# Kernel tuning notes

Measured on AMD Instinct MI355X. Metric: run time of the kernel, lower is better.

The kernel has to match this reference:

```python
import jax, jax.numpy as jnp
import numpy as np

NUM_GRAPHS = 8
N_NODES = 100000


def setup_inputs() -> dict:
    key = jax.random.key(0)
    ks = jax.random.split(key, 8)
    d = 64
    E = 1600000
    x = jax.random.normal(ks[0], (N_NODES, d), dtype=jnp.float32)
    # nn.Linear weights (out,in) with std=0.1 init per GNNlayer; biases zero
    W1 = 0.1 * jax.random.normal(ks[1], (d, d), dtype=jnp.float32)
    W2 = 0.1 * jax.random.normal(ks[2], (d, d), dtype=jnp.float32)
    W3 = 0.1 * jax.random.normal(ks[3], (d, d), dtype=jnp.float32)
    b1 = jnp.zeros((d,), dtype=jnp.float32)
    b2 = jnp.zeros((d,), dtype=jnp.float32)
    b3 = jnp.zeros((d,), dtype=jnp.float32)
    src = jax.random.randint(ks[4], (E,), 0, N_NODES, dtype=jnp.int32)
    dst = jax.random.randint(ks[5], (E,), 0, N_NODES, dtype=jnp.int32)
    node2graph = jnp.sort(jax.random.randint(ks[6], (N_NODES,), 0, NUM_GRAPHS, dtype=jnp.int32))
    return {"x": x, "W1": W1, "b1": b1, "W2": W2, "b2": b2,
            "W3": W3, "b3": b3, "src": src, "dst": dst, "node2graph": node2graph}


def _gnn_layer(h, W, b, src, dst):
    # GNNlayer: per-node linear, then copy_u -> sum reduce at dst
    m = h @ W.T + b                       # [N, d]
    msg = m[src]                          # [E, d] edge gather
    return jax.ops.segment_sum(msg, dst, num_segments=N_NODES)  # [N, d]


def reference(x, W1, b1, W2, b2, W3, b3, src, dst, node2graph):
    h = jnp.tanh(_gnn_layer(x, W1, b1, src, dst))
    h = jnp.tanh(_gnn_layer(h, W2, b2, src, dst))
    H_feat = _gnn_layer(h, W3, b3, src, dst)      # [N, out_dim]
    # dgl.unbatch + per-graph sum of all node features -> scalar per graph
    node_scalar = jnp.sum(H_feat, axis=-1)        # [N]
    per_graph = jax.ops.segment_sum(node_scalar, node2graph, num_segments=NUM_GRAPHS)
    return per_graph[None, :]                     # [1, num_graphs]
```

## Files before the change

kernel.cpp:

```cpp
#include <hip/hip_runtime.h>
#include <math.h>

#define NGRAPHS 8
#define KBSHIFT 8
#define BSZ 256
#define KMAX 512
#define BSTRIDE 6144
#define PCHUNK 3125

typedef _Float16 h2 __attribute__((ext_vector_type(2)));
typedef _Float16 v8hf __attribute__((ext_vector_type(8)));
typedef float f32x4 __attribute__((ext_vector_type(4)));

__device__ __forceinline__ h2 as_h2(unsigned u) { return __builtin_bit_cast(h2, u); }
__device__ __forceinline__ unsigned as_u(h2 h) { return __builtin_bit_cast(unsigned, h); }
__device__ __forceinline__ unsigned pkf16(float a, float b) {
    auto v = __builtin_amdgcn_cvt_pkrtz(a, b);
    return __builtin_bit_cast(unsigned, v);
}
__device__ __forceinline__ float ftanh(float x) {
    float t = __expf(2.0f * x);
    return 1.0f - 2.0f * __builtin_amdgcn_rcpf(t + 1.0f);
}

template<bool TANH, bool INH, bool ZB>
__global__ __launch_bounds__(256) void gemm_kernel(
    const void* __restrict__ in_, const float* __restrict__ W,
    const float* __restrict__ bias, unsigned* __restrict__ out,
    int* __restrict__ bcursor, int N)
{
    __shared__ union {
        struct { uint4 Wc[512]; uint4 Xc[512]; } s;
        float Cf[64 * 68];
    } u;
    const int t = threadIdx.x;
    const int node0 = blockIdx.x * 64;
    if (ZB && blockIdx.x == 0) { bcursor[t] = 0; bcursor[t + 256] = 0; }

    const float4* W4 = (const float4*)W;
    #pragma unroll
    for (int k = 0; k < 2; ++k) {
        int idx = k * 256 + t;
        int o = idx >> 3, ch = idx & 7;
        float4 w0 = W4[idx * 2];
        float4 w1 = W4[idx * 2 + 1];
        u.s.Wc[o * 8 + (ch ^ (o & 7))] =
            make_uint4(pkf16(w0.x, w0.y), pkf16(w0.z, w0.w),
                       pkf16(w1.x, w1.y), pkf16(w1.z, w1.w));
    }
    if (INH) {
        const uint4* in4 = (const uint4*)in_ + (size_t)node0 * 8;
        #pragma unroll
        for (int k = 0; k < 2; ++k) {
            int idx = k * 256 + t;
            int nl = idx >> 3, ch = idx & 7;
            uint4 v = in4[idx];
            h2 p0 = as_h2(v.x), p1 = as_h2(v.y), p2 = as_h2(v.z), p3 = as_h2(v.w);
            float f0 = (float)p0.x, f1 = (float)p0.y, f2 = (float)p1.x, f3 = (float)p1.y;
            float f4 = (float)p2.x, f5 = (float)p2.y, f6 = (float)p3.x, f7 = (float)p3.y;
            if (TANH) {
                f0 = ftanh(f0); f1 = ftanh(f1); f2 = ftanh(f2); f3 = ftanh(f3);
                f4 = ftanh(f4); f5 = ftanh(f5); f6 = ftanh(f6); f7 = ftanh(f7);
            }
            u.s.Xc[nl * 8 + (ch ^ (nl & 7))] =
                make_uint4(pkf16(f0, f1), pkf16(f2, f3), pkf16(f4, f5), pkf16(f6, f7));
        }
    } else {
        const float4* in4 = (const float4*)in_ + (size_t)node0 * 16;
        #pragma unroll
        for (int k = 0; k < 2; ++k) {
            int idx = k * 256 + t;
            int nl = idx >> 3, ch = idx & 7;
            float4 a0 = make_float4(0.f, 0.f, 0.f, 0.f);
            float4 a1 = make_float4(0.f, 0.f, 0.f, 0.f);
            if (node0 + nl < N) { a0 = in4[idx * 2]; a1 = in4[idx * 2 + 1]; }
            if (TANH) {
                a0.x = ftanh(a0.x); a0.y = ftanh(a0.y); a0.z = ftanh(a0.z); a0.w = ftanh(a0.w);
                a1.x = ftanh(a1.x); a1.y = ftanh(a1.y); a1.z = ftanh(a1.z); a1.w = ftanh(a1.w);
            }
            u.s.Xc[nl * 8 + (ch ^ (nl & 7))] =
                make_uint4(pkf16(a0.x, a0.y), pkf16(a0.z, a0.w),
                           pkf16(a1.x, a1.y), pkf16(a1.z, a1.w));
        }
    }
    __syncthreads();

    const int w = t >> 6, l = t & 63;
    const int lo = l & 15, kb = l >> 4, sx = lo & 7;
    const v8hf* Xv = (const v8hf*)u.s.Xc;
    const v8hf* Wv = (const v8hf*)u.s.Wc;
    const int arow = (w * 16 + lo) * 8;
    v8hf a0 = Xv[arow + (kb ^ sx)];
    v8hf a1 = Xv[arow + ((4 + kb) ^ sx)];
    f32x4 acc[4];
    #pragma unroll
    for (int i = 0; i < 4; ++i) acc[i] = (f32x4){0.f, 0.f, 0.f, 0.f};
    #pragma unroll
    for (int ct = 0; ct < 4; ++ct) {
        const int brow = (ct * 16 + lo) * 8;
        v8hf b0 = Wv[brow + (kb ^ sx)];
        v8hf b1 = Wv[brow + ((4 + kb) ^ sx)];
        acc[ct] = __builtin_amdgcn_mfma_f32_16x16x32_f16(a0, b0, acc[ct], 0, 0, 0);
        acc[ct] = __builtin_amdgcn_mfma_f32_16x16x32_f16(a1, b1, acc[ct], 0, 0, 0);
    }
    __syncthreads();

    #pragma unroll
    for (int ct = 0; ct < 4; ++ct) {
        #pragma unroll
        for (int j = 0; j < 4; ++j)
            u.Cf[(w * 16 + kb * 4 + j) * 68 + ct * 16 + lo] = acc[ct][j];
    }
    __syncthreads();

    {
        const int nl = t >> 2, seg = t & 3;
        if (node0 + nl < N) {
            const float* cp = &u.Cf[nl * 68 + seg * 16];
            float4 c0 = *(const float4*)(cp);
            float4 c1 = *(const float4*)(cp + 4);
            float4 c2 = *(const float4*)(cp + 8);
            float4 c3 = *(const float4*)(cp + 12);
            const float4* b4 = (const float4*)bias + seg * 4;
            float4 e0 = b4[0], e1 = b4[1], e2 = b4[2], e3 = b4[3];
            uint4 o0 = make_uint4(pkf16(c0.x + e0.x, c0.y + e0.y), pkf16(c0.z + e0.z, c0.w + e0.w),
                                  pkf16(c1.x + e1.x, c1.y + e1.y), pkf16(c1.z + e1.z, c1.w + e1.w));
            uint4 o1 = make_uint4(pkf16(c2.x + e2.x, c2.y + e2.y), pkf16(c2.z + e2.z, c2.w + e2.w),
                                  pkf16(c3.x + e3.x, c3.y + e3.y), pkf16(c3.z + e3.z, c3.w + e3.w));
            uint4* op = (uint4*)out + (size_t)(node0 + nl) * 8 + seg * 2;
            op[0] = o0;
            op[1] = o1;
        }
    }
}

__global__ __launch_bounds__(512) void partition_kernel(
    const int* __restrict__ src, const int* __restrict__ dst,
    int* __restrict__ bcursor, unsigned* __restrict__ pairs, int E, int K)
{
    __shared__ int h[512];
    __shared__ int sh[512];
    __shared__ int base[512];
    __shared__ int cur[512];
    __shared__ unsigned val[PCHUNK + 3];
    __shared__ unsigned short bk[PCHUNK + 3];
    const int t = threadIdx.x;
    const int lo = blockIdx.x * PCHUNK;
    int hi = lo + PCHUNK; if (hi > E) hi = E;
    const int cnt = hi - lo;

    h[t] = 0; cur[t] = 0;
    __syncthreads();
    for (int e = lo + t; e < hi; e += 512)
        atomicAdd(&h[dst[e] >> KBSHIFT], 1);
    __syncthreads();
    int v = h[t];
    int x = v;
    #pragma unroll
    for (int off = 1; off < 512; off <<= 1) {
        int u = (t >= off) ? h[t - off] : 0;
        __syncthreads();
        x += u;
        h[t] = x;
        __syncthreads();
    }
    sh[t] = x - v;
    base[t] = (t < K && v > 0) ? atomicAdd(&bcursor[t], v) : 0;
    __syncthreads();
    for (int e = lo + t; e < hi; e += 512) {
        int d = dst[e];
        int k = d >> KBSHIFT;
        int pos = atomicAdd(&cur[k], 1);
        int j = sh[k] + pos;
        val[j] = ((unsigned)(d & (BSZ - 1)) << 23) | (unsigned)src[e];
        bk[j] = (unsigned short)k;
    }
    __syncthreads();
    for (int j = t; j < cnt; j += 512) {
        int k = bk[j];
        int idx = base[k] + (j - sh[k]);
        if (idx < BSTRIDE)
            pairs[(size_t)k * BSTRIDE + idx] = val[j];
    }
}

__global__ __launch_bounds__(256) void bucket_build_kernel(
    const unsigned* __restrict__ pairs, const int* __restrict__ bcursor,
    int* __restrict__ rowptr, int* __restrict__ rowend, int* __restrict__ esrc,
    const float* __restrict__ W3, const float* __restrict__ b3,
    float* __restrict__ w3s, int N)
{
    __shared__ int cnt[BSZ];
    __shared__ int tmp[BSZ];
    __shared__ int cur[BSZ];
    const int k = blockIdx.x;
    const int t = threadIdx.x;
    const int ebase = k * BSTRIDE;
    int ec = bcursor[k]; if (ec > BSTRIDE) ec = BSTRIDE;
    const int eend = ebase + ec;

    cnt[t] = 0;
    __syncthreads();
    for (int e = ebase + t; e < eend; e += BSZ)
        atomicAdd(&cnt[pairs[e] >> 23], 1);
    __syncthreads();

    int v = cnt[t];
    tmp[t] = v;
    __syncthreads();
    #pragma unroll
    for (int off = 1; off < BSZ; off <<= 1) {
        int u = (t >= off) ? tmp[t - off] : 0;
        __syncthreads();
        tmp[t] += u;
        __syncthreads();
    }
    int excl = tmp[t] - v;
    cur[t] = excl;
    int n = (k << KBSHIFT) + t;
    if (n < N) {
        rowptr[n] = ebase + excl;
        rowend[n] = ebase + excl + v;
    }
    __syncthreads();

    for (int e = ebase + t; e < eend; e += BSZ) {
        unsigned p = pairs[e];
        int pos = atomicAdd(&cur[p >> 23], 1);
        esrc[ebase + pos] = (int)(p & 0x7fffffu);
    }

    if (k == 0) {
        if (t < 64) {
            float s = 0.f;
            for (int o = 0; o < 64; ++o) s += W3[o * 64 + t];
            w3s[t] = s;
        }
        if (t == 64) {
            float bs = 0.f;
            for (int j = 0; j < 64; ++j) bs += b3[j];
            w3s[64] = bs;
        }
    }
}

__global__ __launch_bounds__(256) void gather_agg_kernel(
    const uint4* __restrict__ m, const int* __restrict__ esrc,
    const int* __restrict__ rowptr, const int* __restrict__ rowend,
    uint4* __restrict__ out, int N)
{
    const int t = threadIdx.x;
    const int n = blockIdx.x * 8 + (t >> 5);
    const int l32 = t & 31;
    const int sub = l32 >> 3, c = l32 & 7;
    h2 a0 = {0, 0}, a1 = {0, 0}, a2 = {0, 0}, a3 = {0, 0};
    if (n < N) {
        int beg = rowptr[n], end = rowend[n];
        int e = beg + sub;
        for (; e + 4 < end; e += 8) {
            int sA = esrc[e], sB = esrc[e + 4];
            uint4 vA = m[(size_t)sA * 8 + c];
            uint4 vB = m[(size_t)sB * 8 + c];
            a0 += as_h2(vA.x); a1 += as_h2(vA.y);
            a2 += as_h2(vA.z); a3 += as_h2(vA.w);
            a0 += as_h2(vB.x); a1 += as_h2(vB.y);
            a2 += as_h2(vB.z); a3 += as_h2(vB.w);
        }
        if (e < end) {
            uint4 vA = m[(size_t)esrc[e] * 8 + c];
            a0 += as_h2(vA.x); a1 += as_h2(vA.y);
            a2 += as_h2(vA.z); a3 += as_h2(vA.w);
        }
    }
    #pragma unroll
    for (int d = 8; d <= 16; d <<= 1) {
        a0 += as_h2(__shfl_xor(as_u(a0), d));
        a1 += as_h2(__shfl_xor(as_u(a1), d));
        a2 += as_h2(__shfl_xor(as_u(a2), d));
        a3 += as_h2(__shfl_xor(as_u(a3), d));
    }
    if (sub == 0 && n < N)
        out[(size_t)n * 8 + c] = make_uint4(as_u(a0), as_u(a1), as_u(a2), as_u(a3));
}

__global__ __launch_bounds__(256) void gather_s3_kernel(
    const uint4* __restrict__ m, const int* __restrict__ esrc,
    const int* __restrict__ rowptr, const int* __restrict__ rowend,
    const float* __restrict__ w3s, float* __restrict__ s3,
    float* __restrict__ outz, int N)
{
    const int t = threadIdx.x;
    if (blockIdx.x == 0 && t < NGRAPHS) outz[t] = 0.f;
    const int n = blockIdx.x * 8 + (t >> 5);
    const int l32 = t & 31;
    const int sub = l32 >> 3, c = l32 & 7;
    h2 a0 = {0, 0}, a1 = {0, 0}, a2 = {0, 0}, a3 = {0, 0};
    if (n < N) {
        int beg = rowptr[n], end = rowend[n];
        int e = beg + sub;
        for (; e + 4 < end; e += 8) {
            int sA = esrc[e], sB = esrc[e + 4];
            uint4 vA = m[(size_t)sA * 8 + c];
            uint4 vB = m[(size_t)sB * 8 + c];
            a0 += as_h2(vA.x); a1 += as_h2(vA.y);
            a2 += as_h2(vA.z); a3 += as_h2(vA.w);
            a0 += as_h2(vB.x); a1 += as_h2(vB.y);
            a2 += as_h2(vB.z); a3 += as_h2(vB.w);
        }
        if (e < end) {
            uint4 vA = m[(size_t)esrc[e] * 8 + c];
            a0 += as_h2(vA.x); a1 += as_h2(vA.y);
            a2 += as_h2(vA.z); a3 += as_h2(vA.w);
        }
    }
    #pragma unroll
    for (int d = 8; d <= 16; d <<= 1) {
        a0 += as_h2(__shfl_xor(as_u(a0), d));
        a1 += as_h2(__shfl_xor(as_u(a1), d));
        a2 += as_h2(__shfl_xor(as_u(a2), d));
        a3 += as_h2(__shfl_xor(as_u(a3), d));
    }
    float4 w0 = ((const float4*)w3s)[c * 2];
    float4 w1 = ((const float4*)w3s)[c * 2 + 1];
    float partial = ftanh((float)a0.x) * w0.x + ftanh((float)a0.y) * w0.y
                  + ftanh((float)a1.x) * w0.z + ftanh((float)a1.y) * w0.w
                  + ftanh((float)a2.x) * w1.x + ftanh((float)a2.y) * w1.y
                  + ftanh((float)a3.x) * w1.z + ftanh((float)a3.y) * w1.w;
    partial += __shfl_xor(partial, 1);
    partial += __shfl_xor(partial, 2);
    partial += __shfl_xor(partial, 4);
    if (l32 == 0 && n < N) s3[n] = partial + w3s[64];
}

__global__ __launch_bounds__(256) void graph_reduce_kernel(
    const float* __restrict__ s3, const int* __restrict__ esrc,
    const int* __restrict__ rowptr, const int* __restrict__ rowend,
    const int* __restrict__ n2g, float* __restrict__ out, int N)
{
    __shared__ float bins[NGRAPHS];
    int t = threadIdx.x;
    if (t < NGRAPHS) bins[t] = 0.f;
    __syncthreads();
    int n = blockIdx.x * 256 + t;
    if (n < N) {
        float acc = 0.f;
        for (int e = rowptr[n]; e < rowend[n]; ++e) acc += s3[esrc[e]];
        atomicAdd(&bins[n2g[n]], acc);
    }
    __syncthreads();
    if (t < NGRAPHS) unsafeAtomicAdd(&out[t], bins[t]);
}

extern "C" void kernel_launch(void* const* d_in, const int* in_sizes, int n_in,
                              void* d_out, int out_size, void* d_ws, size_t ws_size,
                              hipStream_t stream)
{
    const float* x   = (const float*)d_in[0];
    const float* W1  = (const float*)d_in[1];
    const float* b1  = (const float*)d_in[2];
    const float* W2  = (const float*)d_in[3];
    const float* b2  = (const float*)d_in[4];
    const float* W3  = (const float*)d_in[5];
    const float* b3  = (const float*)d_in[6];
    const int*   src = (const int*)d_in[7];
    const int*   dst = (const int*)d_in[8];
    const int*   n2g = (const int*)d_in[9];

    const int N = in_sizes[0] / 64;
    const int E = in_sizes[7];
    const int K = (N + BSZ - 1) >> KBSHIFT;
    const int nb = (N + 255) / 256;

    char* p = (char*)d_ws;
    auto carve = [&](size_t bytes) {
        char* r = p;
        p += (bytes + 255) & ~(size_t)255;
        return r;
    };
    unsigned* A     = (unsigned*)carve((size_t)N * 64 * 2);
    unsigned* B     = (unsigned*)carve((size_t)N * 64 * 2);
    float* s3b      = (float*)carve((size_t)N * sizeof(float));
    float* w3s      = (float*)carve(65 * sizeof(float));
    int*   bcursor  = (int*)carve(KMAX * sizeof(int));
    int*   rowptr   = (int*)carve((size_t)N * sizeof(int));
    int*   rowend   = (int*)carve((size_t)N * sizeof(int));
    int*   esrc     = (int*)carve((size_t)K * BSTRIDE * sizeof(int));
    unsigned* pairs = (unsigned*)B;
    float* out      = (float*)d_out;

    const int gemm_blocks = (N + 63) / 64;
    const int gath_blocks = (N + 7) / 8;
    const int part_blocks = (E + PCHUNK - 1) / PCHUNK;

    gemm_kernel<false, false, true><<<gemm_blocks, 256, 0, stream>>>(x, W1, b1, A, bcursor, N);

    partition_kernel<<<part_blocks, 512, 0, stream>>>(src, dst, bcursor, pairs, E, K);
    bucket_build_kernel<<<K, BSZ, 0, stream>>>(pairs, bcursor, rowptr, rowend,
                                               esrc, W3, b3, w3s, N);

    gather_agg_kernel<<<gath_blocks, 256, 0, stream>>>(
        (const uint4*)A, esrc, rowptr, rowend, (uint4*)B, N);

    gemm_kernel<true, true, false><<<gemm_blocks, 256, 0, stream>>>(B, W2, b2, A, nullptr, N);

    gather_s3_kernel<<<gath_blocks, 256, 0, stream>>>(
        (const uint4*)A, esrc, rowptr, rowend, w3s, s3b, out, N);

    graph_reduce_kernel<<<nb, 256, 0, stream>>>(s3b, esrc, rowptr, rowend, n2g, out, N);
}
```

Baseline: 219.7 us.

## Fuse layer-1 gather-aggregate with layer-2 GEMM and parallelize graph reduce

Merges the edge gather/segment-sum kernel with the following tanh+linear GEMM. Each 64-node block gathers its rows directly into shared memory and then runs the MFMA GEMM, so the fp16 intermediate is never written to and reread from global memory, and one launch is dropped. The final graph reduce now uses 8 lanes per node with shuffle reduction instead of one thread per node. The trade-off is that each fused block processes its 64 nodes in 8 sequential gather rounds, and the grid has fewer blocks than the old gather kernel, which may reduce latency hiding for the random gathers.

```diff
diff --git a/kernel.cpp b/kernel.cpp
--- a/kernel.cpp
+++ b/kernel.cpp
@@ -23,9 +23,9 @@
     return 1.0f - 2.0f * __builtin_amdgcn_rcpf(t + 1.0f);
 }
 
-template<bool TANH, bool INH, bool ZB>
+template<bool TANH, bool ZB>
 __global__ __launch_bounds__(256) void gemm_kernel(
-    const void* __restrict__ in_, const float* __restrict__ W,
+    const float* __restrict__ in_, const float* __restrict__ W,
     const float* __restrict__ bias, unsigned* __restrict__ out,
     int* __restrict__ bcursor, int N)
 {
@@ -48,24 +48,7 @@
             make_uint4(pkf16(w0.x, w0.y), pkf16(w0.z, w0.w),
                        pkf16(w1.x, w1.y), pkf16(w1.z, w1.w));
     }
-    if (INH) {
-        const uint4* in4 = (const uint4*)in_ + (size_t)node0 * 8;
-        #pragma unroll
-        for (int k = 0; k < 2; ++k) {
-            int idx = k * 256 + t;
-            int nl = idx >> 3, ch = idx & 7;
-            uint4 v = in4[idx];
-            h2 p0 = as_h2(v.x), p1 = as_h2(v.y), p2 = as_h2(v.z), p3 = as_h2(v.w);
-            float f0 = (float)p0.x, f1 = (float)p0.y, f2 = (float)p1.x, f3 = (float)p1.y;
-            float f4 = (float)p2.x, f5 = (float)p2.y, f6 = (float)p3.x, f7 = (float)p3.y;
-            if (TANH) {
-                f0 = ftanh(f0); f1 = ftanh(f1); f2 = ftanh(f2); f3 = ftanh(f3);
-                f4 = ftanh(f4); f5 = ftanh(f5); f6 = ftanh(f6); f7 = ftanh(f7);
-            }
-            u.s.Xc[nl * 8 + (ch ^ (nl & 7))] =
-                make_uint4(pkf16(f0, f1), pkf16(f2, f3), pkf16(f4, f5), pkf16(f6, f7));
-        }
-    } else {
+    {
         const float4* in4 = (const float4*)in_ + (size_t)node0 * 16;
         #pragma unroll
         for (int k = 0; k < 2; ++k) {
@@ -134,6 +117,122 @@
     }
 }
 
+__global__ __launch_bounds__(256) void gather_gemm_kernel(
+    const uint4* __restrict__ m, const int* __restrict__ esrc,
+    const int* __restrict__ rowptr, const int* __restrict__ rowend,
+    const float* __restrict__ W, const float* __restrict__ bias,
+    unsigned* __restrict__ out, int N)
+{
+    __shared__ union {
+        struct { uint4 Wc[512]; uint4 Xc[512]; } s;
+        float Cf[64 * 68];
+    } u;
+    const int t = threadIdx.x;
+    const int node0 = blockIdx.x * 64;
+
+    const float4* W4 = (const float4*)W;
+    #pragma unroll
+    for (int k = 0; k < 2; ++k) {
+        int idx = k * 256 + t;
+        int o = idx >> 3, ch = idx & 7;
+        float4 w0 = W4[idx * 2];
+        float4 w1 = W4[idx * 2 + 1];
+        u.s.Wc[o * 8 + (ch ^ (o & 7))] =
+            make_uint4(pkf16(w0.x, w0.y), pkf16(w0.z, w0.w),
+                       pkf16(w1.x, w1.y), pkf16(w1.z, w1.w));
+    }
+
+    const int grp = t >> 5, l32 = t & 31;
+    const int sub = l32 >> 3, c = l32 & 7;
+    for (int i = 0; i < 8; ++i) {
+        const int nl = grp * 8 + i;
+        const int n = node0 + nl;
+        h2 a0 = {0, 0}, a1 = {0, 0}, a2 = {0, 0}, a3 = {0, 0};
+        if (n < N) {
+            int beg = rowptr[n], end = rowend[n];
+            int e = beg + sub;
+            for (; e + 4 < end; e += 8) {
+                int sA = esrc[e], sB = esrc[e + 4];
+                uint4 vA = m[(size_t)sA * 8 + c];
+                uint4 vB = m[(size_t)sB * 8 + c];
+                a0 += as_h2(vA.x); a1 += as_h2(vA.y);
+                a2 += as_h2(vA.z); a3 += as_h2(vA.w);
+                a0 += as_h2(vB.x); a1 += as_h2(vB.y);
+                a2 += as_h2(vB.z); a3 += as_h2(vB.w);
+            }
+            if (e < end) {
+                uint4 vA = m[(size_t)esrc[e] * 8 + c];
+                a0 += as_h2(vA.x); a1 += as_h2(vA.y);
+                a2 += as_h2(vA.z); a3 += as_h2(vA.w);
+            }
+        }
+        #pragma unroll
+        for (int d = 8; d <= 16; d <<= 1) {
+            a0 += as_h2(__shfl_xor(as_u(a0), d));
+            a1 += as_h2(__shfl_xor(as_u(a1), d));
+            a2 += as_h2(__shfl_xor(as_u(a2), d));
+            a3 += as_h2(__shfl_xor(as_u(a3), d));
+        }
+        if (sub == 0) {
+            float f0 = ftanh((float)a0.x), f1 = ftanh((float)a0.y);
+            float f2 = ftanh((float)a1.x), f3 = ftanh((float)a1.y);
+            float f4 = ftanh((float)a2.x), f5 = ftanh((float)a2.y);
+            float f6 = ftanh((float)a3.x), f7 = ftanh((float)a3.y);
+            u.s.Xc[nl * 8 + (c ^ (nl & 7))] =
+                make_uint4(pkf16(f0, f1), pkf16(f2, f3), pkf16(f4, f5), pkf16(f6, f7));
+        }
+    }
+    __syncthreads();
+
+    const int w = t >> 6, l = t & 63;
+    const int lo = l & 15, kb = l >> 4, sx = lo & 7;
+    const v8hf* Xv = (const v8hf*)u.s.Xc;
+    const v8hf* Wv = (const v8hf*)u.s.Wc;
+    const int arow = (w * 16 + lo) * 8;
+    v8hf a0 = Xv[arow + (kb ^ sx)];
+    v8hf a1 = Xv[arow + ((4 + kb) ^ sx)];
+    f32x4 acc[4];
+    #pragma unroll
+    for (int i = 0; i < 4; ++i) acc[i] = (f32x4){0.f, 0.f, 0.f, 0.f};
+    #pragma unroll
+    for (int ct = 0; ct < 4; ++ct) {
+        const int brow = (ct * 16 + lo) * 8;
+        v8hf b0 = Wv[brow + (kb ^ sx)];
+        v8hf b1 = Wv[brow + ((4 + kb) ^ sx)];
+        acc[ct] = __builtin_amdgcn_mfma_f32_16x16x32_f16(a0, b0, acc[ct], 0, 0, 0);
+        acc[ct] = __builtin_amdgcn_mfma_f32_16x16x32_f16(a1, b1, acc[ct], 0, 0, 0);
+    }
+    __syncthreads();
+
+    #pragma unroll
+    for (int ct = 0; ct < 4; ++ct) {
+        #pragma unroll
+        for (int j = 0; j < 4; ++j)
+            u.Cf[(w * 16 + kb * 4 + j) * 68 + ct * 16 + lo] = acc[ct][j];
+    }
+    __syncthreads();
+
+    {
+        const int nl = t >> 2, seg = t & 3;
+        if (node0 + nl < N) {
+            const float* cp = &u.Cf[nl * 68 + seg * 16];
+            float4 c0 = *(const float4*)(cp);
+            float4 c1 = *(const float4*)(cp + 4);
+            float4 c2 = *(const float4*)(cp + 8);
+            float4 c3 = *(const float4*)(cp + 12);
+            const float4* b4 = (const float4*)bias + seg * 4;
+            float4 e0 = b4[0], e1 = b4[1], e2 = b4[2], e3 = b4[3];
+            uint4 o0 = make_uint4(pkf16(c0.x + e0.x, c0.y + e0.y), pkf16(c0.z + e0.z, c0.w + e0.w),
+                                  pkf16(c1.x + e1.x, c1.y + e1.y), pkf16(c1.z + e1.z, c1.w + e1.w));
+            uint4 o1 = make_uint4(pkf16(c2.x + e2.x, c2.y + e2.y), pkf16(c2.z + e2.z, c2.w + e2.w),
+                                  pkf16(c3.x + e3.x, c3.y + e3.y), pkf16(c3.z + e3.z, c3.w + e3.w));
+            uint4* op = (uint4*)out + (size_t)(node0 + nl) * 8 + seg * 2;
+            op[0] = o0;
+            op[1] = o1;
+        }
+    }
+}
+
 __global__ __launch_bounds__(512) void partition_kernel(
     const int* __restrict__ src, const int* __restrict__ dst,
     int* __restrict__ bcursor, unsigned* __restrict__ pairs, int E, int K)
@@ -242,45 +341,6 @@
             w3s[64] = bs;
         }
     }
-}
-
-__global__ __launch_bounds__(256) void gather_agg_kernel(
-    const uint4* __restrict__ m, const int* __restrict__ esrc,
-    const int* __restrict__ rowptr, const int* __restrict__ rowend,
-    uint4* __restrict__ out, int N)
-{
-    const int t = threadIdx.x;
-    const int n = blockIdx.x * 8 + (t >> 5);
-    const int l32 = t & 31;
-    const int sub = l32 >> 3, c = l32 & 7;
-    h2 a0 = {0, 0}, a1 = {0, 0}, a2 = {0, 0}, a3 = {0, 0};
-    if (n < N) {
-        int beg = rowptr[n], end = rowend[n];
-        int e = beg + sub;
-        for (; e + 4 < end; e += 8) {
-            int sA = esrc[e], sB = esrc[e + 4];
-            uint4 vA = m[(size_t)sA * 8 + c];
-            uint4 vB = m[(size_t)sB * 8 + c];
-            a0 += as_h2(vA.x); a1 += as_h2(vA.y);
-            a2 += as_h2(vA.z); a3 += as_h2(vA.w);
-            a0 += as_h2(vB.x); a1 += as_h2(vB.y);
-            a2 += as_h2(vB.z); a3 += as_h2(vB.w);
-        }
-        if (e < end) {
-            uint4 vA = m[(size_t)esrc[e] * 8 + c];
-            a0 += as_h2(vA.x); a1 += as_h2(vA.y);
-            a2 += as_h2(vA.z); a3 += as_h2(vA.w);
-        }
-    }
-    #pragma unroll
-    for (int d = 8; d <= 16; d <<= 1) {
-        a0 += as_h2(__shfl_xor(as_u(a0), d));
-        a1 += as_h2(__shfl_xor(as_u(a1), d));
-        a2 += as_h2(__shfl_xor(as_u(a2), d));
-        a3 += as_h2(__shfl_xor(as_u(a3), d));
-    }
-    if (sub == 0 && n < N)
-        out[(size_t)n * 8 + c] = make_uint4(as_u(a0), as_u(a1), as_u(a2), as_u(a3));
 }
 
 __global__ __launch_bounds__(256) void gather_s3_kernel(
@@ -338,15 +398,20 @@
     const int* __restrict__ n2g, float* __restrict__ out, int N)
 {
     __shared__ float bins[NGRAPHS];
-    int t = threadIdx.x;
+    const int t = threadIdx.x;
     if (t < NGRAPHS) bins[t] = 0.f;
     __syncthreads();
-    int n = blockIdx.x * 256 + t;
+    const int g = t >> 3, c = t & 7;
+    const int n = blockIdx.x * 32 + g;
+    float acc = 0.f;
     if (n < N) {
-        float acc = 0.f;
-        for (int e = rowptr[n]; e < rowend[n]; ++e) acc += s3[esrc[e]];
-        atomicAdd(&bins[n2g[n]], acc);
-    }
+        int beg = rowptr[n], end = rowend[n];
+        for (int e = beg + c; e < end; e += 8) acc += s3[esrc[e]];
+    }
+    acc += __shfl_xor(acc, 1);
+    acc += __shfl_xor(acc, 2);
+    acc += __shfl_xor(acc, 4);
+    if (c == 0 && n < N) atomicAdd(&bins[n2g[n]], acc);
     __syncthreads();
     if (t < NGRAPHS) unsafeAtomicAdd(&out[t], bins[t]);
 }
@@ -369,7 +434,7 @@
     const int N = in_sizes[0] / 64;
     const int E = in_sizes[7];
     const int K = (N + BSZ - 1) >> KBSHIFT;
-    const int nb = (N + 255) / 256;
+    const int nb = (N + 31) / 32;
 
     char* p = (char*)d_ws;
     auto carve = [&](size_t bytes) {
@@ -392,19 +457,17 @@
     const int gath_blocks = (N + 7) / 8;
     const int part_blocks = (E + PCHUNK - 1) / PCHUNK;
 
-    gemm_kernel<false, false, true><<<gemm_blocks, 256, 0, stream>>>(x, W1, b1, A, bcursor, N);
+    gemm_kernel<false, true><<<gemm_blocks, 256, 0, stream>>>(x, W1, b1, A, bcursor, N);
 
     partition_kernel<<<part_blocks, 512, 0, stream>>>(src, dst, bcursor, pairs, E, K);
     bucket_build_kernel<<<K, BSZ, 0, stream>>>(pairs, bcursor, rowptr, rowend,
                                                esrc, W3, b3, w3s, N);
 
-    gather_agg_kernel<<<gath_blocks, 256, 0, stream>>>(
-        (const uint4*)A, esrc, rowptr, rowend, (uint4*)B, N);
-
-    gemm_kernel<true, true, false><<<gemm_blocks, 256, 0, stream>>>(B, W2, b2, A, nullptr, N);
+    gather_gemm_kernel<<<gemm_blocks, 256, 0, stream>>>(
+        (const uint4*)A, esrc, rowptr, rowend, W2, b2, B, N);
 
     gather_s3_kernel<<<gath_blocks, 256, 0, stream>>>(
-        (const uint4*)A, esrc, rowptr, rowend, w3s, s3b, out, N);
+        (const uint4*)B, esrc, rowptr, rowend, w3s, s3b, out, N);
 
     graph_reduce_kernel<<<nb, 256, 0, stream>>>(s3b, esrc, rowptr, rowend, n2g, out, N);
 }
```

After: 242.9 us. 10.5% more time.
